# Kernel optimization log

Hardware: AMD Instinct MI355X
Metric: run time of the kernel (lower is better)

Reference implementation:

```python
import jax, jax.numpy as jnp
import numpy as np

HEADS, KV_HEADS, HEAD_DIM = 32, 8, 64


def apply_rope(x, cos, sin):
    # x: [b,h,s,d], cos/sin: [s, d//2]; pairs are interleaved (even/odd)
    c = cos[None, None, :, :]
    s = sin[None, None, :, :]
    x1 = x[..., 0::2]
    x2 = x[..., 1::2]
    xn = x1 * c - x2 * s
    yn = x1 * s + x2 * c
    return jnp.stack([xn, yn], axis=-1).reshape(x.shape)


def setup_inputs() -> dict:
    key = jax.random.key(0)
    ks = jax.random.split(key, 7)
    b, s, h = 1, 2048, 2048
    return {
        "x": jax.random.normal(ks[0], (b, s, h), jnp.float32),
        "cos": jax.random.normal(ks[1], (s, HEAD_DIM // 2), jnp.float32),
        "sin": jax.random.normal(ks[2], (s, HEAD_DIM // 2), jnp.float32),
        "Wq": jax.random.normal(ks[3], (h, HEADS * HEAD_DIM), jnp.float32) * 0.02,
        "Wk": jax.random.normal(ks[4], (h, KV_HEADS * HEAD_DIM), jnp.float32) * 0.02,
        "Wv": jax.random.normal(ks[5], (h, KV_HEADS * HEAD_DIM), jnp.float32) * 0.02,
        "Wo": jax.random.normal(ks[6], (HEADS * HEAD_DIM, h), jnp.float32) * 0.02,
    }


def reference(x, cos, sin, Wq, Wk, Wv, Wo):
    b, seq, hidden = x.shape
    Q = x @ Wq  # [b,s,H*d]
    K = x @ Wk  # [b,s,Kh*d]
    V = x @ Wv
    q = Q.reshape(b, seq, HEADS, HEAD_DIM).transpose(0, 2, 1, 3)      # b h s d
    k = K.reshape(b, seq, KV_HEADS, HEAD_DIM).transpose(0, 2, 1, 3)   # b k s d
    v = V.reshape(b, seq, KV_HEADS, HEAD_DIM).transpose(0, 2, 1, 3)
    r = HEADS // KV_HEADS
    # einops 'b k s d -> b (r k) s d': tile kv-head block r times
    k = jnp.tile(k, (1, r, 1, 1))
    v = jnp.tile(v, (1, r, 1, 1))
    q = apply_rope(q, cos, sin)
    k = apply_rope(k, cos, sin)
    scale = 1.0 / jnp.sqrt(jnp.float32(HEAD_DIM))
    qk = jnp.einsum('bhqd,bhkd->bhqk', q, k) * scale
    mask = jnp.triu(jnp.full((seq, seq), -jnp.inf, qk.dtype), k=1)
    attn = jax.nn.softmax(qk + mask, axis=-1)
    av = jnp.einsum('bhqk,bhkd->bhqd', attn, v)
    av = av.transpose(0, 2, 1, 3).reshape(b, seq, HEADS * HEAD_DIM)
    return av @ Wo
```

## Files before the change

### kernel.cpp

```cpp
#include <hip/hip_runtime.h>

typedef unsigned short u16;
typedef __attribute__((ext_vector_type(4))) float f32x4;
typedef __attribute__((ext_vector_type(16))) float f32x16;
typedef __attribute__((ext_vector_type(8))) __bf16 bf16x8;
typedef __attribute__((ext_vector_type(2))) __bf16 bf16x2;

#define HEADS 32
#define KV_HEADS 8
#define HD 64
#define SEQ 2048
#define HID 2048
#define NQK 3072
#define QSCALE (0.125f * 1.4426950408889634f)
#define OCH 2097152u

#define AS1 __attribute__((address_space(1)))
#define AS3 __attribute__((address_space(3)))

__device__ __forceinline__ u16 f2bf(float f) {
  unsigned u = __float_as_uint(f);
  u += 0x7FFFu + ((u >> 16) & 1u);
  return (u16)(u >> 16);
}

__device__ __forceinline__ unsigned pk2(float a, float b) {
  union { bf16x2 h; unsigned u; } c;
  c.h[0] = (__bf16)a; c.h[1] = (__bf16)b;
  return c.u;
}

__device__ __forceinline__ float bflo(unsigned u) {
  return __uint_as_float(u << 16);
}
__device__ __forceinline__ float bfhi(unsigned u) {
  return __uint_as_float(u & 0xFFFF0000u);
}

__device__ __forceinline__ void load16_to_lds(const void* g, void* l) {
  __builtin_amdgcn_global_load_lds((AS1 void*)(void*)g, (AS3 void*)l, 16, 0, 0);
}

__global__ __launch_bounds__(256) void k_f2b(const float* __restrict__ in,
                                             u16* __restrict__ out, int n4) {
  int i = blockIdx.x * 256 + threadIdx.x;
  if (i >= n4) return;
  float4 v = ((const float4*)in)[i];
  ushort4 o;
  o.x = f2bf(v.x); o.y = f2bf(v.y); o.z = f2bf(v.z); o.w = f2bf(v.w);
  ((ushort4*)out)[i] = o;
}

__global__ __launch_bounds__(256) void k_tconv(const float* __restrict__ in, int ldi,
                                               u16* __restrict__ out, int ldo) {
  __shared__ float tile[32][33];
  int c0 = blockIdx.x * 32, r0 = blockIdx.y * 32;
  int col = threadIdx.x & 31, rw = threadIdx.x >> 5;
#pragma unroll
  for (int i = 0; i < 4; i++)
    tile[rw + i * 8][col] = in[(size_t)(r0 + rw + i * 8) * ldi + c0 + col];
  __syncthreads();
#pragma unroll
  for (int i = 0; i < 4; i++)
    out[(size_t)(c0 + rw + i * 8) * ldo + r0 + col] = f2bf(tile[col][rw + i * 8]);
}


__device__ __forceinline__ void stage8(const u16* Ap, const u16* Bp, u16* AsX,
                                       u16* BsX, int tid, int K, int koff) {
#pragma unroll
  for (int i = 0; i < 4; i++) {
    load16_to_lds(Ap + (size_t)(i * 32) * K + koff, AsX + (i * 256 + tid) * 8);
    load16_to_lds(Bp + (size_t)(i * 32) * K + koff, BsX + (i * 256 + tid) * 8);
  }
}

__device__ __forceinline__ void frag16(const u16* Asb, const u16* Bsb,
                                       const int aoff[4][2], const int boff[4][2],
                                       f32x4 acc[4][4]) {
#pragma unroll
  for (int kk = 0; kk < 2; kk++) {
    bf16x8 a[4], b[4];
#pragma unroll
    for (int i = 0; i < 4; i++)
      a[i] = *(const bf16x8*)((const char*)Asb + aoff[i][kk]);
#pragma unroll
    for (int j = 0; j < 4; j++)
      b[j] = *(const bf16x8*)((const char*)Bsb + boff[j][kk]);
#pragma unroll
    for (int i = 0; i < 4; i++)
#pragma unroll
      for (int j = 0; j < 4; j++)
        acc[i][j] = __builtin_amdgcn_mfma_f32_16x16x32_bf16(a[i], b[j], acc[i][j], 0, 0, 0);
  }
}

#define TILE_STEP(AsX, BsX, tnext)                              \
  do {                                                          \
    asm volatile("s_waitcnt vmcnt(8)" ::: "memory");            \
    __builtin_amdgcn_sched_barrier(0);                          \
    __builtin_amdgcn_s_barrier();                               \
    frag16(AsX, BsX, aoff, boff, acc);                          \
    __builtin_amdgcn_sched_barrier(0);                          \
    __builtin_amdgcn_s_barrier();                               \
    stage8(Ap, Bp, AsX, BsX, tid, K, (tnext) * 64);             \
    __builtin_amdgcn_sched_barrier(0);                          \
  } while (0)

#define TILE_TAIL(AsX, BsX, n)                                  \
  do {                                                          \
    asm volatile("s_waitcnt vmcnt(" #n ")" ::: "memory");       \
    __builtin_amdgcn_sched_barrier(0);                          \
    __builtin_amdgcn_s_barrier();                               \
    frag16(AsX, BsX, aoff, boff, acc);                          \
  } while (0)

#define GEMM128_PRELUDE(Abase, Bbase)                                          \
  int tid = threadIdx.x;                                                       \
  int m0 = blockIdx.x * 128, n0 = blockIdx.y * 128;                            \
  int l = tid & 63, w = tid >> 6;                                              \
  int lr = l & 15, lg = l >> 4;                                                \
  int wr = (w >> 1) * 64, wc = (w & 1) * 64;                                   \
  f32x4 acc[4][4] = {};                                                        \
  int r8 = tid >> 3;                                                           \
  int sx = (tid & 7) ^ (r8 & 7);                                               \
  const u16* Ap = (Abase) + (size_t)(m0 + r8) * K + sx * 8;                    \
  const u16* Bp = (Bbase) + (size_t)(n0 + r8) * K + sx * 8;                    \
  int aoff[4][2], boff[4][2];                                                  \
  _Pragma("unroll") for (int i = 0; i < 4; i++) {                              \
    int ra = wr + i * 16 + lr;                                                 \
    int rb = wc + i * 16 + lr;                                                 \
    _Pragma("unroll") for (int kk = 0; kk < 2; kk++) {                         \
      aoff[i][kk] = ra * 128 + (((lg + kk * 4) ^ (ra & 7)) << 4);              \
      boff[i][kk] = rb * 128 + (((lg + kk * 4) ^ (rb & 7)) << 4);              \
    }                                                                          \
  }                                                                            \
  stage8(Ap, Bp, As0, Bs0, tid, K, 0);                                         \
  stage8(Ap, Bp, As1, Bs1, tid, K, 64);                                        \
  _Pragma("unroll 1") for (int t = 0; t < 30; t += 2) {                        \
    TILE_STEP(As0, Bs0, t + 2);                                                \
    TILE_STEP(As1, Bs1, t + 3);                                                \
  }                                                                            \
  TILE_TAIL(As0, Bs0, 8);                                                      \
  TILE_TAIL(As1, Bs1, 0);

__global__ __launch_bounds__(256) void k_gemm(const u16* __restrict__ A,
                                              const u16* __restrict__ Bt,
                                              float* __restrict__ C,
                                              int M, int N, int K) {
  __shared__ u16 smem[32768];
  u16* As0 = smem;          u16* As1 = smem + 8192;
  u16* Bs0 = smem + 16384;  u16* Bs1 = smem + 24576;
  GEMM128_PRELUDE(A, Bt)

#pragma unroll
  for (int i = 0; i < 4; i++)
#pragma unroll
    for (int j = 0; j < 4; j++)
#pragma unroll
      for (int r = 0; r < 4; r++)
        C[(size_t)(m0 + wr + i * 16 + lg * 4 + r) * N + n0 + wc + j * 16 + lr] =
            acc[i][j][r];
}

__global__ __launch_bounds__(256) void k_gemm_qkv(const u16* __restrict__ A,
                                                  const u16* __restrict__ Bt,
                                                  const float* __restrict__ cosp,
                                                  const float* __restrict__ sinp,
                                                  u16* __restrict__ qbuf,
                                                  u16* __restrict__ kbuf,
                                                  u16* __restrict__ vtb) {
  __shared__ u16 smem[32768];
  u16* As0 = smem;          u16* As1 = smem + 8192;
  u16* Bs0 = smem + 16384;  u16* Bs1 = smem + 24576;
  u16* Ts = smem;
  const int K = HID;
  GEMM128_PRELUDE(A, Bt)

  if (n0 < 2560) {
    int colbase = n0 + wc;
    bool isQ = colbase < 2048;
    float scale = isQ ? QSCALE : 1.0f;
    u16* base = isQ ? qbuf + (size_t)(colbase >> 6) * SEQ * HD
                    : kbuf + (size_t)((colbase - 2048) >> 6) * SEQ * HD;
    int odd = lr & 1;
#pragma unroll
    for (int i = 0; i < 4; i++)
#pragma unroll
      for (int j = 0; j < 4; j++) {
        int ii = j * 8 + (lr >> 1);
#pragma unroll
        for (int r = 0; r < 4; r++) {
          float v = acc[i][j][r];
          float vp = __shfl_xor(v, 1, 64);
          int sr = m0 + wr + i * 16 + lg * 4 + r;
          float cs = cosp[sr * 32 + ii], sn = sinp[sr * 32 + ii];
          float x1 = odd ? vp : v, x2 = odd ? v : vp;
          float o = odd ? (x1 * sn + x2 * cs) : (x1 * cs - x2 * sn);
          base[(size_t)sr * HD + j * 16 + lr] = f2bf(o * scale);
        }
      }
  } else {
    __syncthreads();
#pragma unroll
    for (int i = 0; i < 4; i++)
#pragma unroll
      for (int j = 0; j < 4; j++)
#pragma unroll
        for (int r = 0; r < 4; r++) {
          int cB = wc + j * 16 + lr, rB = wr + i * 16 + lg * 4 + r;
          *(u16*)((char*)Ts + cB * 256 + ((rB * 2) ^ ((cB & 7) << 4))) =
              f2bf(acc[i][j][r]);
        }
    __syncthreads();
    int c = tid >> 1, half = tid & 1;
    int col = n0 + c;
    int kvh = (col - 2560) >> 6, d = col & 63;
    u16* dst = vtb + (size_t)kvh * HD * SEQ + (size_t)d * SEQ + m0 + half * 64;
    const char* src = (const char*)Ts + c * 256;
    int cs7 = (c & 7) << 4;
#pragma unroll
    for (int q = 0; q < 8; q++)
      *(uint4*)(dst + q * 8) = *(const uint4*)(src + ((half * 128 + q * 16) ^ cs7));
  }
}

__global__ __launch_bounds__(256) void k_flash2(const u16* __restrict__ qb,
                                                const u16* __restrict__ kb,
                                                const u16* __restrict__ vt,
                                                unsigned* __restrict__ Opart,
                                                float2* __restrict__ ml) {
  __shared__ u16 Ks[2][64 * 64];
  __shared__ u16 Vs[2][64 * 64];
  int bid = blockIdx.x;
  int c = bid & 1;
  int b5 = bid >> 1;
  int h = b5 & 31;
  int qi = b5 >> 5;
  int qblk = (SEQ / 128) - 1 - qi;
  int kvh = h & 7;
  int tid = threadIdx.x, w = tid >> 6, l = tid & 63;
  int lq = l & 31, hi = l >> 5;
  const u16* qh = qb + (size_t)h * SEQ * HD;
  const u16* kh = kb + (size_t)kvh * SEQ * HD;
  const u16* vh = vt + (size_t)kvh * HD * SEQ;
  int wq0 = qblk * 128 + w * 32;
  int qg = wq0 + lq;

  bf16x8 qf[4];
#pragma unroll
  for (int ds = 0; ds < 4; ds++)
    qf[ds] = *(const bf16x8*)(qh + (size_t)qg * HD + ds * 16 + hi * 8);

  f32x16 acc[2] = {};
  float m_r = -__builtin_inff(), l_r = 0.f;

  int srow = tid >> 2, c4 = tid & 3, swz = (srow & 7) << 4;
  int sd0 = srow * 128 + ((c4 * 32) ^ swz);
  int sd1 = srow * 128 + ((c4 * 32 + 16) ^ swz);
  const int kt0 = c * (qblk + 1), kt1 = kt0 + qblk + 1;

  {
    const u16* ksrc = kh + (size_t)(kt0 * 64 + srow) * HD + c4 * 16;
    const u16* vsrc = vh + (size_t)srow * SEQ + kt0 * 64 + c4 * 16;
    uint4 a0 = *(const uint4*)(ksrc), a1 = *(const uint4*)(ksrc + 8);
    uint4 b0 = *(const uint4*)(vsrc), b1 = *(const uint4*)(vsrc + 8);
    *(uint4*)((char*)Ks[0] + sd0) = a0; *(uint4*)((char*)Ks[0] + sd1) = a1;
    *(uint4*)((char*)Vs[0] + sd0) = b0; *(uint4*)((char*)Vs[0] + sd1) = b1;
  }
  __syncthreads();

  uint4 kr0, kr1, vr0, vr1;
  int lswz = (lq & 7) << 4;
  for (int kt = kt0; kt < kt1; kt++) {
    int b = (kt - kt0) & 1;
    if (kt + 1 < kt1) {
      const u16* ksrc = kh + (size_t)((kt + 1) * 64 + srow) * HD + c4 * 16;
      const u16* vsrc = vh + (size_t)srow * SEQ + (kt + 1) * 64 + c4 * 16;
      kr0 = *(const uint4*)(ksrc); kr1 = *(const uint4*)(ksrc + 8);
      vr0 = *(const uint4*)(vsrc); vr1 = *(const uint4*)(vsrc + 8);
    }

    if (kt * 64 <= wq0 + 31) {
      f32x16 sT[2] = {};
      const char* kbase = (const char*)Ks[b];
      __builtin_amdgcn_s_setprio(1);
#pragma unroll
      for (int t = 0; t < 2; t++) {
#pragma unroll
        for (int ds = 0; ds < 4; ds++) {
          bf16x8 kf = *(const bf16x8*)(kbase + (t * 32 + lq) * 128 +
                                       ((ds * 32 + hi * 16) ^ lswz));
          sT[t] = __builtin_amdgcn_mfma_f32_32x32x16_bf16(kf, qf[ds], sT[t], 0, 0, 0);
        }
      }
      __builtin_amdgcn_s_setprio(0);

      if (kt * 64 + 63 > wq0) {
#pragma unroll
        for (int t = 0; t < 2; t++)
#pragma unroll
          for (int r = 0; r < 16; r++) {
            int kg = kt * 64 + t * 32 + (r & 3) + 8 * (r >> 2) + 4 * hi;
            if (kg > qg) sT[t][r] = -__builtin_inff();
          }
      }

      float pmax = sT[0][0];
#pragma unroll
      for (int r = 1; r < 16; r++) pmax = fmaxf(pmax, sT[0][r]);
#pragma unroll
      for (int r = 0; r < 16; r++) pmax = fmaxf(pmax, sT[1][r]);
      pmax = fmaxf(pmax, __shfl_xor(pmax, 32, 64));

      if (!__all(pmax <= m_r + 8.f)) {
        float mn = fmaxf(m_r, pmax);
        float scl = __builtin_amdgcn_exp2f(m_r - mn);
        l_r *= scl;
        acc[0] *= scl;
        acc[1] *= scl;
        m_r = mn;
      }

      float ss = 0.f;
#pragma unroll
      for (int t = 0; t < 2; t++)
#pragma unroll
        for (int r = 0; r < 16; r++) {
          float p = __builtin_amdgcn_exp2f(sT[t][r] - m_r);
          sT[t][r] = p;
          ss += p;
        }
      ss += __shfl_xor(ss, 32, 64);
      l_r += ss;

      const char* vbase = (const char*)Vs[b];
#pragma unroll
      for (int t = 0; t < 2; t++) {
        unsigned cp[4][2];
#pragma unroll
        for (int m = 0; m < 4; m++) {
          cp[m][0] = pk2(sT[t][4 * m + 0], sT[t][4 * m + 1]);
          cp[m][1] = pk2(sT[t][4 * m + 2], sT[t][4 * m + 3]);
        }
#pragma unroll
        for (int kl = 0; kl < 2; kl++) {
          unsigned s0 = hi ? cp[2 * kl][0] : cp[2 * kl + 1][0];
          unsigned s1 = hi ? cp[2 * kl][1] : cp[2 * kl + 1][1];
          unsigned r0 = (unsigned)__shfl_xor((int)s0, 32, 64);
          unsigned r1 = (unsigned)__shfl_xor((int)s1, 32, 64);
          union { unsigned u[4]; bf16x8 v; } pa;
          pa.u[0] = hi ? r0 : cp[2 * kl][0];
          pa.u[1] = hi ? r1 : cp[2 * kl][1];
          pa.u[2] = hi ? cp[2 * kl + 1][0] : r0;
          pa.u[3] = hi ? cp[2 * kl + 1][1] : r1;
          int ks = t * 2 + kl;
          __builtin_amdgcn_s_setprio(1);
#pragma unroll
          for (int dt = 0; dt < 2; dt++) {
            bf16x8 vb = *(const bf16x8*)(vbase + (dt * 32 + lq) * 128 +
                                         ((ks * 32 + hi * 16) ^ lswz));
            acc[dt] = __builtin_amdgcn_mfma_f32_32x32x16_bf16(vb, pa.v, acc[dt], 0, 0, 0);
          }
          __builtin_amdgcn_s_setprio(0);
        }
      }
    }

    if (kt + 1 < kt1) {
      *(uint4*)((char*)Ks[b ^ 1] + sd0) = kr0;
      *(uint4*)((char*)Ks[b ^ 1] + sd1) = kr1;
      *(uint4*)((char*)Vs[b ^ 1] + sd0) = vr0;
      *(uint4*)((char*)Vs[b ^ 1] + sd1) = vr1;
    }
    __syncthreads();
  }

  unsigned* op = Opart + (size_t)c * OCH + ((size_t)(b5 * 4 + w) * 16) * 64;
#pragma unroll
  for (int dt = 0; dt < 2; dt++)
#pragma unroll
    for (int j = 0; j < 8; j++)
      op[(dt * 8 + j) * 64 + l] = pk2(acc[dt][2 * j], acc[dt][2 * j + 1]);
  if (!hi)
    ml[c * (HEADS * SEQ) + h * SEQ + wq0 + lq] = make_float2(m_r, l_r);
}

__global__ __launch_bounds__(256) void k_merge(const unsigned* __restrict__ Opart,
                                               const float2* __restrict__ ml,
                                               u16* __restrict__ av) {
  __shared__ u16 Ts[8192];
  int bid = blockIdx.x;
  int h = bid & 31, qblk = bid >> 5;
  int b5 = ((SEQ / 128 - 1 - qblk) << 5) | h;
  int tid = threadIdx.x, w = tid >> 6, l = tid & 63;
  int lq = l & 31, hi = l >> 5;
  int wq0 = qblk * 128 + w * 32;

  float2 ml0 = ml[h * SEQ + wq0 + lq];
  float2 ml1 = ml[HEADS * SEQ + h * SEQ + wq0 + lq];
  float m = fmaxf(ml0.x, ml1.x);
  float f0 = __builtin_amdgcn_exp2f(ml0.x - m);
  float f1 = __builtin_amdgcn_exp2f(ml1.x - m);
  float inv = 1.0f / (ml0.y * f0 + ml1.y * f1);

  const unsigned* op0 = Opart + ((size_t)(b5 * 4 + w) * 16) * 64;
  const unsigned* op1 = op0 + OCH;
  f32x16 acc[2];
#pragma unroll
  for (int dt = 0; dt < 2; dt++)
#pragma unroll
    for (int j = 0; j < 8; j++) {
      unsigned a0 = op0[(dt * 8 + j) * 64 + l];
      unsigned a1 = op1[(dt * 8 + j) * 64 + l];
      acc[dt][2 * j] = bflo(a0) * f0 + bflo(a1) * f1;
      acc[dt][2 * j + 1] = bfhi(a0) * f0 + bfhi(a1) * f1;
    }

  int lswz = (lq & 7) << 4;
  char* wbase = (char*)Ts + w * 4096;
#pragma unroll
  for (int dt = 0; dt < 2; dt++)
#pragma unroll
    for (int m4 = 0; m4 < 4; m4++) {
      int r0 = 4 * m4;
      uint2 pr;
      pr.x = pk2(acc[dt][r0 + 0] * inv, acc[dt][r0 + 1] * inv);
      pr.y = pk2(acc[dt][r0 + 2] * inv, acc[dt][r0 + 3] * inv);
      int byte = lq * 128 + ((dt * 64 + m4 * 16 + hi * 8) ^ lswz);
      *(uint2*)(wbase + byte) = pr;
    }
  __syncthreads();
  int q2 = l >> 1, cH = l & 1;
  int qswz = (q2 & 7) << 4;
#pragma unroll
  for (int i = 0; i < 4; i++) {
    uint4 d = *(const uint4*)(wbase + q2 * 128 + ((cH * 64 + i * 16) ^ qswz));
    *(uint4*)(av + (size_t)(wq0 + q2) * HID + h * HD + cH * 32 + i * 8) = d;
  }
}

extern "C" void kernel_launch(void* const* d_in, const int* in_sizes, int n_in,
                              void* d_out, int out_size, void* d_ws, size_t ws_size,
                              hipStream_t stream) {
  (void)in_sizes; (void)n_in; (void)out_size; (void)ws_size;
  const float* x = (const float*)d_in[0];
  const float* cosp = (const float*)d_in[1];
  const float* sinp = (const float*)d_in[2];
  const float* Wq = (const float*)d_in[3];
  const float* Wk = (const float*)d_in[4];
  const float* Wv = (const float*)d_in[5];
  const float* Wo = (const float*)d_in[6];
  float* out = (float*)d_out;
  char* ws = (char*)d_ws;

  u16* xb = (u16*)(ws);
  float2* mlb = (float2*)(ws);
  u16* Wqkv = (u16*)(ws + ((size_t)8 << 20));
  u16* WoT = (u16*)(ws + ((size_t)20 << 20));
  u16* qbuf = (u16*)(ws + ((size_t)28 << 20));
  u16* kbuf = (u16*)(ws + ((size_t)36 << 20));
  u16* vtb = (u16*)(ws + ((size_t)38 << 20));
  u16* av = (u16*)(ws + ((size_t)40 << 20));
  unsigned* Opart = (unsigned*)(ws + ((size_t)48 << 20));

  k_f2b<<<(SEQ * HID / 4 + 255) / 256, 256, 0, stream>>>(x, xb, SEQ * HID / 4);
  k_tconv<<<dim3(HID / 32, HID / 32), 256, 0, stream>>>(Wq, HID, Wqkv, HID);
  k_tconv<<<dim3(512 / 32, HID / 32), 256, 0, stream>>>(Wk, 512, Wqkv + (size_t)2048 * HID, HID);
  k_tconv<<<dim3(512 / 32, HID / 32), 256, 0, stream>>>(Wv, 512, Wqkv + (size_t)2560 * HID, HID);
  k_tconv<<<dim3(HID / 32, HID / 32), 256, 0, stream>>>(Wo, HID, WoT, HID);
  k_gemm_qkv<<<dim3(SEQ / 128, NQK / 128), 256, 0, stream>>>(xb, Wqkv, cosp, sinp,
                                                             qbuf, kbuf, vtb);
  k_flash2<<<(SEQ / 128) * HEADS * 2, 256, 0, stream>>>(qbuf, kbuf, vtb, Opart, mlb);
  k_merge<<<(SEQ / 128) * HEADS, 256, 0, stream>>>(Opart, mlb, av);
  k_gemm<<<dim3(SEQ / 128, HID / 128), 256, 0, stream>>>(av, WoT, out, SEQ, HID, HID);
}
```

Measured before the change: 125.6 us.

## Switch GEMM mainloop to 4-stage K=32 LDS pipeline with prioritized MFMA

```diff
diff --git a/kernel.cpp b/kernel.cpp
--- a/kernel.cpp
+++ b/kernel.cpp
@@ -66,53 +66,48 @@
 }
 
 
-__device__ __forceinline__ void stage8(const u16* Ap, const u16* Bp, u16* AsX,
+__device__ __forceinline__ void stage4(const u16* Ap, const u16* Bp, u16* AsX,
                                        u16* BsX, int tid, int K, int koff) {
-#pragma unroll
-  for (int i = 0; i < 4; i++) {
-    load16_to_lds(Ap + (size_t)(i * 32) * K + koff, AsX + (i * 256 + tid) * 8);
-    load16_to_lds(Bp + (size_t)(i * 32) * K + koff, BsX + (i * 256 + tid) * 8);
-  }
-}
-
-__device__ __forceinline__ void frag16(const u16* Asb, const u16* Bsb,
-                                       const int aoff[4][2], const int boff[4][2],
-                                       f32x4 acc[4][4]) {
-#pragma unroll
-  for (int kk = 0; kk < 2; kk++) {
-    bf16x8 a[4], b[4];
-#pragma unroll
-    for (int i = 0; i < 4; i++)
-      a[i] = *(const bf16x8*)((const char*)Asb + aoff[i][kk]);
-#pragma unroll
-    for (int j = 0; j < 4; j++)
-      b[j] = *(const bf16x8*)((const char*)Bsb + boff[j][kk]);
-#pragma unroll
-    for (int i = 0; i < 4; i++)
-#pragma unroll
-      for (int j = 0; j < 4; j++)
-        acc[i][j] = __builtin_amdgcn_mfma_f32_16x16x32_bf16(a[i], b[j], acc[i][j], 0, 0, 0);
-  }
-}
-
-#define TILE_STEP(AsX, BsX, tnext)                              \
-  do {                                                          \
-    asm volatile("s_waitcnt vmcnt(8)" ::: "memory");            \
-    __builtin_amdgcn_sched_barrier(0);                          \
-    __builtin_amdgcn_s_barrier();                               \
-    frag16(AsX, BsX, aoff, boff, acc);                          \
-    __builtin_amdgcn_sched_barrier(0);                          \
-    __builtin_amdgcn_s_barrier();                               \
-    stage8(Ap, Bp, AsX, BsX, tid, K, (tnext) * 64);             \
-    __builtin_amdgcn_sched_barrier(0);                          \
+  load16_to_lds(Ap + koff, AsX + tid * 8);
+  load16_to_lds(Ap + (size_t)64 * K + koff, AsX + 2048 + tid * 8);
+  load16_to_lds(Bp + koff, BsX + tid * 8);
+  load16_to_lds(Bp + (size_t)64 * K + koff, BsX + 2048 + tid * 8);
+}
+
+#define PH_MFMA16()                                                   \
+  __builtin_amdgcn_s_setprio(1);                                      \
+  _Pragma("unroll") for (int i = 0; i < 4; i++)                       \
+      _Pragma("unroll") for (int j = 0; j < 4; j++)                   \
+          acc[i][j] = __builtin_amdgcn_mfma_f32_16x16x32_bf16(        \
+              a_[i], b_[j], acc[i][j], 0, 0, 0);                      \
+  __builtin_amdgcn_s_setprio(0);
+
+#define PH_FULL(Ar, Br, Ad, Bd, pnext)                                \
+  do {                                                                \
+    asm volatile("s_waitcnt vmcnt(8)" ::: "memory");                  \
+    __builtin_amdgcn_sched_barrier(0);                                \
+    __builtin_amdgcn_s_barrier();                                     \
+    bf16x8 a_[4], b_[4];                                              \
+    _Pragma("unroll") for (int i = 0; i < 4; i++) {                   \
+      a_[i] = *(const bf16x8*)((const char*)(Ar) + aoff[i]);          \
+      b_[i] = *(const bf16x8*)((const char*)(Br) + boff[i]);          \
+    }                                                                 \
+    stage4(Ap, Bp, Ad, Bd, tid, K, (pnext) * 32);                     \
+    __builtin_amdgcn_sched_barrier(0);                                \
+    PH_MFMA16()                                                       \
   } while (0)
 
-#define TILE_TAIL(AsX, BsX, n)                                  \
-  do {                                                          \
-    asm volatile("s_waitcnt vmcnt(" #n ")" ::: "memory");       \
-    __builtin_amdgcn_sched_barrier(0);                          \
-    __builtin_amdgcn_s_barrier();                               \
-    frag16(AsX, BsX, aoff, boff, acc);                          \
+#define PH_TAIL(Ar, Br, vm)                                           \
+  do {                                                                \
+    asm volatile("s_waitcnt vmcnt(" #vm ")" ::: "memory");            \
+    __builtin_amdgcn_sched_barrier(0);                                \
+    __builtin_amdgcn_s_barrier();                                     \
+    bf16x8 a_[4], b_[4];                                              \
+    _Pragma("unroll") for (int i = 0; i < 4; i++) {                   \
+      a_[i] = *(const bf16x8*)((const char*)(Ar) + aoff[i]);          \
+      b_[i] = *(const bf16x8*)((const char*)(Br) + boff[i]);          \
+    }                                                                 \
+    PH_MFMA16()                                                       \
   } while (0)
 
 #define GEMM128_PRELUDE(Abase, Bbase)                                          \
@@ -122,35 +117,39 @@
   int lr = l & 15, lg = l >> 4;                                                \
   int wr = (w >> 1) * 64, wc = (w & 1) * 64;                                   \
   f32x4 acc[4][4] = {};                                                        \
-  int r8 = tid >> 3;                                                           \
-  int sx = (tid & 7) ^ (r8 & 7);                                               \
+  int r8 = tid >> 2;                                                           \
+  int sx = (tid & 3) ^ (r8 & 3);                                               \
   const u16* Ap = (Abase) + (size_t)(m0 + r8) * K + sx * 8;                    \
   const u16* Bp = (Bbase) + (size_t)(n0 + r8) * K + sx * 8;                    \
-  int aoff[4][2], boff[4][2];                                                  \
+  int aoff[4], boff[4];                                                        \
   _Pragma("unroll") for (int i = 0; i < 4; i++) {                              \
-    int ra = wr + i * 16 + lr;                                                 \
-    int rb = wc + i * 16 + lr;                                                 \
-    _Pragma("unroll") for (int kk = 0; kk < 2; kk++) {                         \
-      aoff[i][kk] = ra * 128 + (((lg + kk * 4) ^ (ra & 7)) << 4);              \
-      boff[i][kk] = rb * 128 + (((lg + kk * 4) ^ (rb & 7)) << 4);              \
-    }                                                                          \
+    int ra = wr + i * 16 + lr, rb = wc + i * 16 + lr;                          \
+    aoff[i] = ra * 64 + ((lg ^ (ra & 3)) << 4);                                \
+    boff[i] = rb * 64 + ((lg ^ (rb & 3)) << 4);                                \
   }                                                                            \
-  stage8(Ap, Bp, As0, Bs0, tid, K, 0);                                         \
-  stage8(Ap, Bp, As1, Bs1, tid, K, 64);                                        \
-  _Pragma("unroll 1") for (int t = 0; t < 30; t += 2) {                        \
-    TILE_STEP(As0, Bs0, t + 2);                                                \
-    TILE_STEP(As1, Bs1, t + 3);                                                \
+  stage4(Ap, Bp, As0, Bs0, tid, K, 0);                                         \
+  stage4(Ap, Bp, As1, Bs1, tid, K, 32);                                        \
+  stage4(Ap, Bp, As2, Bs2, tid, K, 64);                                        \
+  _Pragma("unroll 1") for (int t = 0; t < 60; t += 4) {                        \
+    PH_FULL(As0, Bs0, As3, Bs3, t + 3);                                        \
+    PH_FULL(As1, Bs1, As0, Bs0, t + 4);                                        \
+    PH_FULL(As2, Bs2, As1, Bs1, t + 5);                                        \
+    PH_FULL(As3, Bs3, As2, Bs2, t + 6);                                        \
   }                                                                            \
-  TILE_TAIL(As0, Bs0, 8);                                                      \
-  TILE_TAIL(As1, Bs1, 0);
+  PH_FULL(As0, Bs0, As3, Bs3, 63);                                             \
+  PH_TAIL(As1, Bs1, 8);                                                        \
+  PH_TAIL(As2, Bs2, 4);                                                        \
+  PH_TAIL(As3, Bs3, 0);
 
 __global__ __launch_bounds__(256) void k_gemm(const u16* __restrict__ A,
                                               const u16* __restrict__ Bt,
                                               float* __restrict__ C,
                                               int M, int N, int K) {
   __shared__ u16 smem[32768];
-  u16* As0 = smem;          u16* As1 = smem + 8192;
-  u16* Bs0 = smem + 16384;  u16* Bs1 = smem + 24576;
+  u16* As0 = smem;          u16* As1 = smem + 4096;
+  u16* As2 = smem + 8192;   u16* As3 = smem + 12288;
+  u16* Bs0 = smem + 16384;  u16* Bs1 = smem + 20480;
+  u16* Bs2 = smem + 24576;  u16* Bs3 = smem + 28672;
   GEMM128_PRELUDE(A, Bt)
 
 #pragma unroll
@@ -171,8 +170,10 @@
                                                   u16* __restrict__ kbuf,
                                                   u16* __restrict__ vtb) {
   __shared__ u16 smem[32768];
-  u16* As0 = smem;          u16* As1 = smem + 8192;
-  u16* Bs0 = smem + 16384;  u16* Bs1 = smem + 24576;
+  u16* As0 = smem;          u16* As1 = smem + 4096;
+  u16* As2 = smem + 8192;   u16* As3 = smem + 12288;
+  u16* Bs0 = smem + 16384;  u16* Bs1 = smem + 20480;
+  u16* Bs2 = smem + 24576;  u16* Bs3 = smem + 28672;
   u16* Ts = smem;
   const int K = HID;
   GEMM128_PRELUDE(A, Bt)
```

After: 130.9 us. 4.2% more time.

## Load QKV GEMM B operand directly into registers, stage only A in LDS

Applied to the files above, without the earlier changes.

```diff
diff --git a/kernel.cpp b/kernel.cpp
--- a/kernel.cpp
+++ b/kernel.cpp
@@ -115,35 +115,6 @@
     frag16(AsX, BsX, aoff, boff, acc);                          \
   } while (0)
 
-#define GEMM128_PRELUDE(Abase, Bbase)                                          \
-  int tid = threadIdx.x;                                                       \
-  int m0 = blockIdx.x * 128, n0 = blockIdx.y * 128;                            \
-  int l = tid & 63, w = tid >> 6;                                              \
-  int lr = l & 15, lg = l >> 4;                                                \
-  int wr = (w >> 1) * 64, wc = (w & 1) * 64;                                   \
-  f32x4 acc[4][4] = {};                                                        \
-  int r8 = tid >> 3;                                                           \
-  int sx = (tid & 7) ^ (r8 & 7);                                               \
-  const u16* Ap = (Abase) + (size_t)(m0 + r8) * K + sx * 8;                    \
-  const u16* Bp = (Bbase) + (size_t)(n0 + r8) * K + sx * 8;                    \
-  int aoff[4][2], boff[4][2];                                                  \
-  _Pragma("unroll") for (int i = 0; i < 4; i++) {                              \
-    int ra = wr + i * 16 + lr;                                                 \
-    int rb = wc + i * 16 + lr;                                                 \
-    _Pragma("unroll") for (int kk = 0; kk < 2; kk++) {                         \
-      aoff[i][kk] = ra * 128 + (((lg + kk * 4) ^ (ra & 7)) << 4);              \
-      boff[i][kk] = rb * 128 + (((lg + kk * 4) ^ (rb & 7)) << 4);              \
-    }                                                                          \
-  }                                                                            \
-  stage8(Ap, Bp, As0, Bs0, tid, K, 0);                                         \
-  stage8(Ap, Bp, As1, Bs1, tid, K, 64);                                        \
-  _Pragma("unroll 1") for (int t = 0; t < 30; t += 2) {                        \
-    TILE_STEP(As0, Bs0, t + 2);                                                \
-    TILE_STEP(As1, Bs1, t + 3);                                                \
-  }                                                                            \
-  TILE_TAIL(As0, Bs0, 8);                                                      \
-  TILE_TAIL(As1, Bs1, 0);
-
 __global__ __launch_bounds__(256) void k_gemm(const u16* __restrict__ A,
                                               const u16* __restrict__ Bt,
                                               float* __restrict__ C,
@@ -151,7 +122,36 @@
   __shared__ u16 smem[32768];
   u16* As0 = smem;          u16* As1 = smem + 8192;
   u16* Bs0 = smem + 16384;  u16* Bs1 = smem + 24576;
-  GEMM128_PRELUDE(A, Bt)
+  int tid = threadIdx.x;
+  int m0 = blockIdx.x * 128, n0 = blockIdx.y * 128;
+  int l = tid & 63, w = tid >> 6;
+  int lr = l & 15, lg = l >> 4;
+  int wr = (w >> 1) * 64, wc = (w & 1) * 64;
+  f32x4 acc[4][4] = {};
+  int r8 = tid >> 3;
+  int sx = (tid & 7) ^ (r8 & 7);
+  const u16* Ap = A + (size_t)(m0 + r8) * K + sx * 8;
+  const u16* Bp = Bt + (size_t)(n0 + r8) * K + sx * 8;
+  int aoff[4][2], boff[4][2];
+#pragma unroll
+  for (int i = 0; i < 4; i++) {
+    int ra = wr + i * 16 + lr;
+    int rb = wc + i * 16 + lr;
+#pragma unroll
+    for (int kk = 0; kk < 2; kk++) {
+      aoff[i][kk] = ra * 128 + (((lg + kk * 4) ^ (ra & 7)) << 4);
+      boff[i][kk] = rb * 128 + (((lg + kk * 4) ^ (rb & 7)) << 4);
+    }
+  }
+  stage8(Ap, Bp, As0, Bs0, tid, K, 0);
+  stage8(Ap, Bp, As1, Bs1, tid, K, 64);
+#pragma unroll 1
+  for (int t = 0; t < 30; t += 2) {
+    TILE_STEP(As0, Bs0, t + 2);
+    TILE_STEP(As1, Bs1, t + 3);
+  }
+  TILE_TAIL(As0, Bs0, 8);
+  TILE_TAIL(As1, Bs1, 0);
 
 #pragma unroll
   for (int i = 0; i < 4; i++)
@@ -162,6 +162,47 @@
         C[(size_t)(m0 + wr + i * 16 + lg * 4 + r) * N + n0 + wc + j * 16 + lr] =
             acc[i][j][r];
 }
+
+
+__device__ __forceinline__ void stageA4(const u16* Ap, u16* AsX, int tid, int K,
+                                        int koff) {
+#pragma unroll
+  for (int i = 0; i < 4; i++)
+    load16_to_lds(Ap + (size_t)(i * 32) * K + koff, AsX + (i * 256 + tid) * 8);
+}
+
+#define QKV_LOADB(BQ, kt)                                                     \
+  _Pragma("unroll") for (int j = 0; j < 4; j++)                               \
+  _Pragma("unroll") for (int kk = 0; kk < 2; kk++)                            \
+      BQ[j * 2 + kk] =                                                        \
+          *(const bf16x8*)(Bgl + (size_t)(j * 16) * K + (kt) * 64 + kk * 32);
+
+#define QKV_COMP(AsR, BQ)                                                     \
+  {                                                                           \
+    bf16x8 a_[4][2];                                                          \
+    _Pragma("unroll") for (int i = 0; i < 4; i++)                             \
+    _Pragma("unroll") for (int kk = 0; kk < 2; kk++)                          \
+        a_[i][kk] = *(const bf16x8*)((const char*)(AsR) + aoff[i][kk]);       \
+    __builtin_amdgcn_s_setprio(1);                                            \
+    _Pragma("unroll") for (int kk = 0; kk < 2; kk++)                          \
+    _Pragma("unroll") for (int i = 0; i < 4; i++)                             \
+    _Pragma("unroll") for (int j = 0; j < 4; j++)                             \
+        acc[i][j] = __builtin_amdgcn_mfma_f32_16x16x32_bf16(                  \
+            a_[i][kk], BQ[j * 2 + kk], acc[i][j], 0, 0, 0);                   \
+    __builtin_amdgcn_s_setprio(0);                                            \
+  }
+
+#define QKV_IT(AsR, AsW, BQc, BQn, tnext)                                     \
+  do {                                                                        \
+    asm volatile("s_waitcnt vmcnt(8)" ::: "memory");                          \
+    __builtin_amdgcn_sched_barrier(0);                                        \
+    __builtin_amdgcn_s_barrier();                                             \
+    stageA4(Ap, AsW, tid, K, (tnext) * 64);                                   \
+    __builtin_amdgcn_sched_barrier(0);                                        \
+    QKV_COMP(AsR, BQc)                                                        \
+    QKV_LOADB(BQn, tnext)                                                     \
+    __builtin_amdgcn_sched_barrier(0);                                        \
+  } while (0)
 
 __global__ __launch_bounds__(256) void k_gemm_qkv(const u16* __restrict__ A,
                                                   const u16* __restrict__ Bt,
@@ -170,12 +211,43 @@
                                                   u16* __restrict__ qbuf,
                                                   u16* __restrict__ kbuf,
                                                   u16* __restrict__ vtb) {
-  __shared__ u16 smem[32768];
-  u16* As0 = smem;          u16* As1 = smem + 8192;
-  u16* Bs0 = smem + 16384;  u16* Bs1 = smem + 24576;
+  __shared__ u16 smem[16384];
+  u16* As0 = smem;
+  u16* As1 = smem + 8192;
   u16* Ts = smem;
   const int K = HID;
-  GEMM128_PRELUDE(A, Bt)
+  int tid = threadIdx.x;
+  int m0 = blockIdx.x * 128, n0 = blockIdx.y * 128;
+  int l = tid & 63, w = tid >> 6;
+  int lr = l & 15, lg = l >> 4;
+  int wr = (w >> 1) * 64, wc = (w & 1) * 64;
+  f32x4 acc[4][4] = {};
+  int r8 = tid >> 3;
+  int sx = (tid & 7) ^ (r8 & 7);
+  const u16* Ap = A + (size_t)(m0 + r8) * K + sx * 8;
+  const u16* Bgl = Bt + (size_t)(n0 + wc + lr) * K + lg * 8;
+  int aoff[4][2];
+#pragma unroll
+  for (int i = 0; i < 4; i++) {
+    int ra = wr + i * 16 + lr;
+#pragma unroll
+    for (int kk = 0; kk < 2; kk++)
+      aoff[i][kk] = ra * 128 + (((lg + kk * 4) ^ (ra & 7)) << 4);
+  }
+
+  bf16x8 bq0[8], bq1[8];
+  stageA4(Ap, As0, tid, K, 0);
+  QKV_LOADB(bq0, 0)
+#pragma unroll 1
+  for (int t = 0; t < 30; t += 2) {
+    QKV_IT(As0, As1, bq0, bq1, t + 1);
+    QKV_IT(As1, As0, bq1, bq0, t + 2);
+  }
+  QKV_IT(As0, As1, bq0, bq1, 31);
+  asm volatile("s_waitcnt vmcnt(8)" ::: "memory");
+  __builtin_amdgcn_sched_barrier(0);
+  __builtin_amdgcn_s_barrier();
+  QKV_COMP(As1, bq1)
 
   if (n0 < 2560) {
     int colbase = n0 + wc;
```

After: 163.8 us. 30.4% more time.
